# Optimization experiments

Measured on AMD Instinct MI355X. Metric: run time of the kernel, lower is better.

## Reference

```python
import jax, jax.numpy as jnp
import numpy as np
from jax import lax

DN = ('NCHW', 'OIHW', 'NCHW')
POOL = 8
TEMP = 1.0
TOP_K = 2
GN1_GROUPS = 8   # get_safe_groups(256, 8)
GN2_GROUPS = 4   # get_safe_groups(16, 4)
EPS = 1e-5


def group_norm(x, gamma, beta, groups):
    B, C, H, W = x.shape
    xg = x.reshape(B, groups, C // groups, H, W)
    mu = xg.mean(axis=(2, 3, 4), keepdims=True)
    var = xg.var(axis=(2, 3, 4), keepdims=True)
    xg = (xg - mu) * lax.rsqrt(var + EPS)
    x = xg.reshape(B, C, H, W)
    return x * gamma[None, :, None, None] + beta[None, :, None, None]


def setup_inputs() -> dict:
    key = jax.random.key(0)
    ks = jax.random.split(key, 6)
    B, C, H, W = 16, 256, 256, 256
    R, E = 16, 8  # reduced_channels = max(256//16, 4), num_experts
    return {
        "x": jax.random.normal(ks[0], (B, C, H, W), jnp.float32),
        "w_dw": jax.random.normal(ks[1], (C, 1, 3, 3), jnp.float32) * 0.1,   # depthwise 3x3
        "gn1_g": jnp.ones((C,), jnp.float32),
        "gn1_b": jnp.zeros((C,), jnp.float32),
        "w_pw1": jax.random.normal(ks[2], (R, C, 1, 1), jnp.float32) * 0.05,  # pointwise C->R
        "gn2_g": jnp.ones((R,), jnp.float32),
        "gn2_b": jnp.zeros((R,), jnp.float32),
        "w_pw2": jax.random.normal(ks[3], (E, R, 1, 1), jnp.float32) * 0.1,   # pointwise R->E
        "b_pw2": jnp.zeros((E,), jnp.float32),
    }


def reference(x, w_dw, gn1_g, gn1_b, w_pw1, gn2_g, gn2_b, w_pw2, b_pw2):
    B, C, H, W = x.shape
    xd = x.reshape(B, C, H // POOL, POOL, W // POOL, POOL).mean(axis=(3, 5))
    # depthwise 3x3, padding=1
    h = lax.conv_general_dilated(xd, w_dw, (1, 1), 'SAME',
                                 feature_group_count=C, dimension_numbers=DN)
    h = jax.nn.silu(group_norm(h, gn1_g, gn1_b, GN1_GROUPS))
    # pointwise C->R
    h = lax.conv_general_dilated(h, w_pw1, (1, 1), 'VALID', dimension_numbers=DN)
    h = jax.nn.silu(group_norm(h, gn2_g, gn2_b, GN2_GROUPS))
    # pointwise R->E with bias
    logits = lax.conv_general_dilated(h, w_pw2, (1, 1), 'VALID', dimension_numbers=DN)
    logits = logits + b_pw2[None, :, None, None]
    # eval path: softmax over experts, spatial mean, top-k, renormalize
    weights = jax.nn.softmax(logits / TEMP, axis=1)       # [B, E, h, w]
    pooled = weights.mean(axis=(2, 3))                    # [B, E]
    topk_vals, topk_idx = lax.top_k(pooled, TOP_K)        # [B, k]
    topk_vals = topk_vals / (topk_vals.sum(axis=1, keepdims=True) + 1e-9)
    return topk_vals[:, :, None, None], topk_idx[:, :, None, None]
```

## Files before the change

### kernel.cpp

```cpp
#include <hip/hip_runtime.h>
#include <hip/hip_bf16.h>
#include <math.h>


#define C_    256
#define HWIN  256
#define OHW   32
#define NPIX  1024
#define R_    16
#define E_    8

using f4 = __attribute__((ext_vector_type(4))) float;

__global__ __launch_bounds__(256) void k1_pool_dw(
    const float* __restrict__ x, const float* __restrict__ wdw,
    float* __restrict__ h1, float* __restrict__ ch_sum,
    float* __restrict__ ch_sumsq) {
  const int bc   = blockIdx.x;
  const int c    = bc & (C_ - 1);
  const int tid  = threadIdx.x;
  const int wv   = tid >> 6, lane = tid & 63;
  const float* plane = x + (size_t)bc * (HWIN * HWIN);

  __shared__ float sm[OHW][OHW + 1];

#pragma unroll
  for (int k = 0; k < 8; ++k) {
    const int pr = wv * 8 + k;
    const float* rp = plane + (size_t)pr * 8 * HWIN + lane * 4;
    float s = 0.f;
#pragma unroll
    for (int r = 0; r < 8; ++r) {
      const f4 a = __builtin_nontemporal_load(
          reinterpret_cast<const f4*>(rp + (size_t)r * HWIN));
      s += (a.x + a.y) + (a.z + a.w);
    }
    s += __shfl_xor(s, 1);
    if (!(lane & 1)) sm[pr][lane >> 1] = s * (1.f / 64.f);
  }

  float w[9];
#pragma unroll
  for (int i = 0; i < 9; ++i) w[i] = wdw[c * 9 + i];
  __syncthreads();

  float ls = 0.f, lss = 0.f;
  for (int p = tid; p < NPIX; p += 256) {
    const int oh = p >> 5, ow = p & 31;
    float acc = 0.f;
#pragma unroll
    for (int ky = 0; ky < 3; ++ky) {
      const int y = oh + ky - 1;
      if ((unsigned)y >= OHW) continue;
#pragma unroll
      for (int kx = 0; kx < 3; ++kx) {
        const int xx = ow + kx - 1;
        if ((unsigned)xx >= OHW) continue;
        acc += w[ky * 3 + kx] * sm[y][xx];
      }
    }
    h1[(size_t)bc * NPIX + p] = acc;
    ls += acc; lss += acc * acc;
  }

#pragma unroll
  for (int m = 32; m >= 1; m >>= 1) {
    ls  += __shfl_xor(ls, m);
    lss += __shfl_xor(lss, m);
  }
  __shared__ float r2[4][2];
  if (lane == 0) { r2[wv][0] = ls; r2[wv][1] = lss; }
  __syncthreads();
  if (tid == 0) {
    ch_sum[bc]   = (r2[0][0] + r2[1][0]) + (r2[2][0] + r2[3][0]);
    ch_sumsq[bc] = (r2[0][1] + r2[1][1]) + (r2[2][1] + r2[3][1]);
  }
}

__global__ __launch_bounds__(256) void k2_pw1(
    const float* __restrict__ h1, const float* __restrict__ ch_sum,
    const float* __restrict__ ch_sumsq, const float* __restrict__ g1,
    const float* __restrict__ b1, const float* __restrict__ w1,
    float* __restrict__ h2, float* __restrict__ st2) {
  const int blk = blockIdx.x;
  const int b   = blk >> 4, q = blk & 15;
  const int tid = threadIdx.x;
  const int wv  = tid >> 6, lane = tid & 63;

  __shared__ float musr[8][2];
  __shared__ float sc[C_], sh[C_];
  __shared__ float w1s[R_ * C_];
  __shared__ float red[4][64][R_ + 1];

  {
    float cs  = ch_sum[b * C_ + tid];
    float css = ch_sumsq[b * C_ + tid];
#pragma unroll
    for (int m = 16; m >= 1; m >>= 1) {
      cs  += __shfl_xor(cs, m);
      css += __shfl_xor(css, m);
    }
    if ((tid & 31) == 0) {
      const int g = tid >> 5;
      const float mu  = cs * (1.f / 32768.f);
      const float var = css * (1.f / 32768.f) - mu * mu;
      musr[g][0] = mu;
      musr[g][1] = rsqrtf(var + 1e-5f);
    }
  }
  for (int i = tid; i < R_ * C_; i += 256) w1s[i] = w1[i];
  __syncthreads();

  {
    const int g = tid >> 5;
    const float mu = musr[g][0], rs = musr[g][1];
    const float ga = g1[tid];
    sc[tid] = rs * ga;
    sh[tid] = b1[tid] - mu * rs * ga;
  }
  __syncthreads();

  const int hw = q * 64 + lane;
  const float* hp = h1 + (size_t)b * C_ * NPIX + hw;
  const int c0 = wv * 64;
  float acc[R_];
#pragma unroll
  for (int r = 0; r < R_; ++r) acc[r] = 0.f;

#pragma unroll 8
  for (int j = 0; j < 64; ++j) {
    const int cc = c0 + j;
    const float v = hp[(size_t)cc * NPIX];
    const float u = v * sc[cc] + sh[cc];
    const float t = u / (1.f + __expf(-u));
#pragma unroll
    for (int r = 0; r < R_; ++r) acc[r] += t * w1s[r * C_ + cc];
  }

#pragma unroll
  for (int r = 0; r < R_; ++r) red[wv][lane][r] = acc[r];
  __syncthreads();

  const int p = tid >> 2, g = tid & 3;
  float gs = 0.f, gss = 0.f;
  float* h2p = h2 + (size_t)b * R_ * NPIX + q * 64 + p;
#pragma unroll
  for (int j = 0; j < 4; ++j) {
    const int r = g * 4 + j;
    const float v = (red[0][p][r] + red[1][p][r]) + (red[2][p][r] + red[3][p][r]);
    h2p[r * NPIX] = v;
    gs += v; gss += v * v;
  }
#pragma unroll
  for (int m = 4; m <= 32; m <<= 1) {
    gs  += __shfl_xor(gs, m);
    gss += __shfl_xor(gss, m);
  }
  __shared__ float red2[4][4][2];
  if (lane < 4) { red2[wv][lane][0] = gs; red2[wv][lane][1] = gss; }
  __syncthreads();
  if (tid < 8) {
    const int gg = tid >> 1, which = tid & 1;
    st2[blk * 8 + tid] = (red2[0][gg][which] + red2[1][gg][which]) +
                         (red2[2][gg][which] + red2[3][gg][which]);
  }
}

__global__ __launch_bounds__(256) void k3_route(
    const float* __restrict__ h2, const float* __restrict__ st2,
    const float* __restrict__ g2, const float* __restrict__ b2,
    const float* __restrict__ w2, const float* __restrict__ bias2,
    float* __restrict__ out) {
  const int b   = blockIdx.x;
  const int tid = threadIdx.x;

  __shared__ float musr[4][2];
  __shared__ float sc2[R_], sh2[R_];
  __shared__ float w2s[E_ * R_ + E_];

  if (tid < 4) {
    float s = 0.f, ss = 0.f;
    for (int qq = 0; qq < 16; ++qq) {
      s  += st2[(b * 16 + qq) * 8 + tid * 2];
      ss += st2[(b * 16 + qq) * 8 + tid * 2 + 1];
    }
    const float mu  = s * (1.f / 4096.f);
    const float var = ss * (1.f / 4096.f) - mu * mu;
    musr[tid][0] = mu;
    musr[tid][1] = rsqrtf(var + 1e-5f);
  }
  if (tid < E_ * R_) w2s[tid] = w2[tid];
  else if (tid < E_ * R_ + E_) w2s[tid] = bias2[tid - E_ * R_];
  __syncthreads();
  if (tid < R_) {
    const int g = tid >> 2;
    const float ga = g2[tid];
    sc2[tid] = musr[g][1] * ga;
    sh2[tid] = b2[tid] - musr[g][0] * musr[g][1] * ga;
  }
  __syncthreads();

  float wa[E_];
#pragma unroll
  for (int e = 0; e < E_; ++e) wa[e] = 0.f;
  const float* hp = h2 + (size_t)b * R_ * NPIX;

  for (int pp = 0; pp < 4; ++pp) {
    const int hw = pp * 256 + tid;
    float t[R_];
#pragma unroll
    for (int r = 0; r < R_; ++r) {
      const float u = hp[r * NPIX + hw] * sc2[r] + sh2[r];
      t[r] = u / (1.f + __expf(-u));
    }
    float lg[E_];
    float mx = -1e30f;
#pragma unroll
    for (int e = 0; e < E_; ++e) {
      float s = w2s[E_ * R_ + e];
#pragma unroll
      for (int r = 0; r < R_; ++r) s += w2s[e * R_ + r] * t[r];
      lg[e] = s;
      mx = fmaxf(mx, s);
    }
    float den = 0.f;
#pragma unroll
    for (int e = 0; e < E_; ++e) { lg[e] = __expf(lg[e] - mx); den += lg[e]; }
    const float inv = 1.f / den;
#pragma unroll
    for (int e = 0; e < E_; ++e) wa[e] += lg[e] * inv;
  }

#pragma unroll
  for (int m = 32; m >= 1; m >>= 1) {
#pragma unroll
    for (int e = 0; e < E_; ++e) wa[e] += __shfl_xor(wa[e], m);
  }
  __shared__ float red[4][E_];
  const int wv = tid >> 6;
  if ((tid & 63) == 0) {
#pragma unroll
    for (int e = 0; e < E_; ++e) red[wv][e] = wa[e];
  }
  __syncthreads();
  __shared__ float pooled[E_];
  if (tid < E_)
    pooled[tid] = ((red[0][tid] + red[1][tid]) + (red[2][tid] + red[3][tid])) * (1.f / 1024.f);
  __syncthreads();

  if (tid == 0) {
    float pv[E_];
#pragma unroll
    for (int e = 0; e < E_; ++e) pv[e] = pooled[e];
    int i1 = 0; float v1 = pv[0];
    for (int e = 1; e < E_; ++e) if (pv[e] > v1) { v1 = pv[e]; i1 = e; }
    pv[i1] = -1e30f;
    int i2 = 0; float v2 = pv[0];
    for (int e = 1; e < E_; ++e) if (pv[e] > v2) { v2 = pv[e]; i2 = e; }
    const float inv = 1.f / (v1 + v2 + 1e-9f);
    out[b * 2 + 0] = v1 * inv;
    out[b * 2 + 1] = v2 * inv;
    out[32 + b * 2 + 0] = (float)i1;
    out[32 + b * 2 + 1] = (float)i2;
  }
}

extern "C" void kernel_launch(void* const* d_in, const int* in_sizes, int n_in,
                              void* d_out, int out_size, void* d_ws, size_t ws_size,
                              hipStream_t stream) {
  const float* x     = (const float*)d_in[0];
  const float* wdw   = (const float*)d_in[1];
  const float* g1    = (const float*)d_in[2];
  const float* b1    = (const float*)d_in[3];
  const float* w1    = (const float*)d_in[4];
  const float* g2    = (const float*)d_in[5];
  const float* b2    = (const float*)d_in[6];
  const float* w2    = (const float*)d_in[7];
  const float* bias2 = (const float*)d_in[8];
  float* out = (float*)d_out;

  char* ws = (char*)d_ws;
  float* h1       = (float*)ws;
  float* h2       = (float*)(ws + (size_t)16 * 1024 * 1024);
  float* ch_sum   = (float*)(ws + (size_t)17 * 1024 * 1024);
  float* ch_sumsq = ch_sum + 4096;
  float* st2      = ch_sumsq + 4096;

  hipLaunchKernelGGL(k1_pool_dw, dim3(16 * C_), dim3(256), 0, stream,
                     x, wdw, h1, ch_sum, ch_sumsq);
  hipLaunchKernelGGL(k2_pw1, dim3(256), dim3(256), 0, stream,
                     h1, ch_sum, ch_sumsq, g1, b1, w1, h2, st2);
  hipLaunchKernelGGL(k3_route, dim3(16), dim3(256), 0, stream,
                     h2, st2, g2, b2, w2, bias2, out);
}
```

Measured before the change: 231.5 us.

## Stream pooling input through LDS ring buffer with async global_load_lds

Replaces the direct nontemporal global loads in the pooling stage with a 3-slot LDS ring fed by global_load_lds, so upcoming chunks of rows are fetched while the current chunk is reduced. Each chunk of 8 rows is summed across waves through a small partial buffer and written one step later. The goal is more loads in flight per block on a memory-bound 256 MB read. In exchange it adds LDS traffic, two barriers per chunk and a larger LDS footprint, which may lower occupancy compared with the plain load path that already had many independent loads.

```diff
diff --git a/kernel.cpp b/kernel.cpp
--- a/kernel.cpp
+++ b/kernel.cpp
@@ -10,7 +10,16 @@
 #define R_    16
 #define E_    8
 
+#define CHUNK_F 2048
+#define NCHUNK  32
+#define RING    3
+
 using f4 = __attribute__((ext_vector_type(4))) float;
+
+#define GLD_LDS16(g, l)                                              \
+  __builtin_amdgcn_global_load_lds(                                  \
+      (const __attribute__((address_space(1))) void*)(g),            \
+      (__attribute__((address_space(3))) void*)(l), 16, 0, 2 )
 
 __global__ __launch_bounds__(256) void k1_pool_dw(
     const float* __restrict__ x, const float* __restrict__ wdw,
@@ -22,26 +31,61 @@
   const int wv   = tid >> 6, lane = tid & 63;
   const float* plane = x + (size_t)bc * (HWIN * HWIN);
 
-  __shared__ float sm[OHW][OHW + 1];
-
-#pragma unroll
-  for (int k = 0; k < 8; ++k) {
-    const int pr = wv * 8 + k;
-    const float* rp = plane + (size_t)pr * 8 * HWIN + lane * 4;
-    float s = 0.f;
-#pragma unroll
-    for (int r = 0; r < 8; ++r) {
-      const f4 a = __builtin_nontemporal_load(
-          reinterpret_cast<const f4*>(rp + (size_t)r * HWIN));
-      s += (a.x + a.y) + (a.z + a.w);
-    }
-    s += __shfl_xor(s, 1);
-    if (!(lane & 1)) sm[pr][lane >> 1] = s * (1.f / 64.f);
-  }
+  __shared__ __attribute__((aligned(16))) float slots[RING][CHUNK_F];
+  __shared__ float wpart[2][4][32];
+  __shared__ float pooled[OHW][OHW + 1];
+  __shared__ float r2[4][2];
 
   float w[9];
 #pragma unroll
   for (int i = 0; i < 9; ++i) w[i] = wdw[c * 9 + i];
+
+#define STAGE(t)                                                        \
+  do {                                                                  \
+    const float* g0 = plane + (size_t)(t) * CHUNK_F + wv * 512 + lane * 4; \
+    float* l0 = &slots[(t) % RING][wv * 512];                           \
+    GLD_LDS16(g0, l0);                                                  \
+    GLD_LDS16(g0 + 256, l0 + 256);                                      \
+  } while (0)
+
+  STAGE(0);
+  STAGE(1);
+
+#pragma unroll 1
+  for (int t = 0; t < NCHUNK; ++t) {
+    __builtin_amdgcn_s_barrier();
+    if (t + 2 < NCHUNK) {
+      STAGE(t + 2);
+      asm volatile("s_waitcnt vmcnt(4)" ::: "memory");
+    } else if (t + 1 < NCHUNK) {
+      asm volatile("s_waitcnt vmcnt(2)" ::: "memory");
+    } else {
+      asm volatile("s_waitcnt vmcnt(0)" ::: "memory");
+    }
+    __builtin_amdgcn_s_barrier();
+
+    {
+      const f4* sf = (const f4*)&slots[t % RING][0];
+      const f4 v0 = sf[tid];
+      const f4 v1 = sf[tid + 256];
+      float s = ((v0.x + v0.y) + (v0.z + v0.w)) +
+                ((v1.x + v1.y) + (v1.z + v1.w));
+      s += __shfl_xor(s, 1);
+      if (!(lane & 1)) wpart[t & 1][wv][lane >> 1] = s;
+      if (t > 0 && tid < 32) {
+        const int pa = (t - 1) & 1;
+        pooled[t - 1][tid] =
+            ((wpart[pa][0][tid] + wpart[pa][1][tid]) +
+             (wpart[pa][2][tid] + wpart[pa][3][tid])) * (1.f / 64.f);
+      }
+    }
+  }
+  __builtin_amdgcn_s_barrier();
+  if (tid < 32) {
+    pooled[NCHUNK - 1][tid] =
+        ((wpart[1][0][tid] + wpart[1][1][tid]) +
+         (wpart[1][2][tid] + wpart[1][3][tid])) * (1.f / 64.f);
+  }
   __syncthreads();
 
   float ls = 0.f, lss = 0.f;
@@ -56,7 +100,7 @@
       for (int kx = 0; kx < 3; ++kx) {
         const int xx = ow + kx - 1;
         if ((unsigned)xx >= OHW) continue;
-        acc += w[ky * 3 + kx] * sm[y][xx];
+        acc += w[ky * 3 + kx] * pooled[y][xx];
       }
     }
     h1[(size_t)bc * NPIX + p] = acc;
@@ -68,13 +112,13 @@
     ls  += __shfl_xor(ls, m);
     lss += __shfl_xor(lss, m);
   }
-  __shared__ float r2[4][2];
   if (lane == 0) { r2[wv][0] = ls; r2[wv][1] = lss; }
   __syncthreads();
   if (tid == 0) {
     ch_sum[bc]   = (r2[0][0] + r2[1][0]) + (r2[2][0] + r2[3][0]);
     ch_sumsq[bc] = (r2[0][1] + r2[1][1]) + (r2[2][1] + r2[3][1]);
   }
+#undef STAGE
 }
 
 __global__ __launch_bounds__(256) void k2_pw1(
```

After: 234.7 us. No clear change (+1.4%).
